# Performance work log

Hardware: AMD Instinct MI355X
Metric: run time of the kernel (lower is better)

## Reference

```python
import jax, jax.numpy as jnp
import numpy as np

B, L, X, Y, A = 32, 1024, 1024, 1024, 16


def setup_inputs() -> dict:
    key = jax.random.key(0)
    ks = jax.random.split(key, 6)
    stdv = 1.0 / np.sqrt(X)
    stdv_h = 1.0 / np.sqrt(Y)
    return {
        "x": jax.random.normal(ks[0], (B, L, X), dtype=jnp.float32),
        "y": jax.random.normal(ks[1], (B, Y), dtype=jnp.float32),
        "x_mask": jnp.zeros((B, L), dtype=bool),
        "actions": jax.random.randint(ks[2], (B,), 0, A),
        "weight": jax.random.uniform(ks[3], (Y, X), minval=-stdv, maxval=stdv, dtype=jnp.float32),
        "bias": jnp.zeros((X,), dtype=jnp.float32),
        "wa_h": jax.random.uniform(ks[4], (A, Y, 1), minval=-stdv_h, maxval=stdv_h, dtype=jnp.float32),
    }


def reference(x, y, x_mask, actions, weight, bias, wa_h):
    # Per-action column scores: softmax over x_size of sum_y(weight * wa_h[a])
    # (equivalent to the torch loop: a2 = weight*wa_h[a]; softmax(a2.sum(0)))
    score2 = jax.nn.softmax(jnp.einsum("yx,ay->ax", weight, wa_h[:, :, 0]), axis=-1)  # [A, X]
    # u[b,a,:] = y[b] @ (weight * score2[a]) = (y@weight)[b] * score2[a];
    # the one-hot mask then selects row actions[b] -> gather instead of A GEMMs.
    yW = y @ weight                                   # [B, X]
    Wy = yW * score2[actions] + bias                  # [B, X]
    xWy = jnp.einsum("blx,bx->bl", x, Wy)             # [B, L]
    xWy = jnp.where(x_mask, -jnp.inf, xWy)
    return jax.nn.log_softmax(xWy, axis=-1)  # training mode
```

## Files before the change

### kernel.cpp

```cpp
#include <hip/hip_runtime.h>
#include <hip/hip_bf16.h>
#include <math.h>

constexpr int Ac = 16;
constexpr int Bc = 32;
constexpr int Lc = 1024;
constexpr int Xc = 1024;
constexpr int Yc = 1024;

__device__ __forceinline__ float waveReduceSum(float v) {
#pragma unroll
    for (int off = 32; off > 0; off >>= 1) v += __shfl_down(v, off, 64);
    return v;
}

__device__ __forceinline__ float waveReduceMax(float v) {
#pragma unroll
    for (int off = 32; off > 0; off >>= 1) v = fmaxf(v, __shfl_down(v, off, 64));
    return v;
}

__global__ __launch_bounds__(256) void k1_proj(
        const float* __restrict__ weight, const float* __restrict__ yv,
        const float* __restrict__ wa_h, float* __restrict__ s_raw,
        float* __restrict__ yW) {
    const int x  = blockIdx.x * 256 + threadIdx.x;
    const int y0 = blockIdx.y * 64;

    float accA[Ac];
    float accB[Bc];
#pragma unroll
    for (int a = 0; a < Ac; ++a) accA[a] = 0.0f;
#pragma unroll
    for (int b = 0; b < Bc; ++b) accB[b] = 0.0f;

    for (int yy = 0; yy < 64; ++yy) {
        const int yi = y0 + yy;
        const float w = weight[(size_t)yi * Xc + x];
#pragma unroll
        for (int a = 0; a < Ac; ++a) accA[a] = fmaf(w, wa_h[a * Yc + yi], accA[a]);
#pragma unroll
        for (int b = 0; b < Bc; ++b) accB[b] = fmaf(w, yv[b * Yc + yi], accB[b]);
    }

#pragma unroll
    for (int a = 0; a < Ac; ++a) atomicAdd(&s_raw[a * Xc + x], accA[a]);
#pragma unroll
    for (int b = 0; b < Bc; ++b) atomicAdd(&yW[b * Xc + x], accB[b]);
}

__global__ __launch_bounds__(256) void k2_softmax(
        const float* __restrict__ s_raw, float* __restrict__ score2) {
    const int a    = blockIdx.x;
    const int tid  = threadIdx.x;
    const int wave = tid >> 6;
    const int lane = tid & 63;
    __shared__ float smax[4];
    __shared__ float ssum[4];

    float v[4];
    float mx = -INFINITY;
#pragma unroll
    for (int k = 0; k < 4; ++k) {
        v[k] = s_raw[a * Xc + tid + k * 256];
        mx = fmaxf(mx, v[k]);
    }
    mx = waveReduceMax(mx);
    if (lane == 0) smax[wave] = mx;
    __syncthreads();
    mx = fmaxf(fmaxf(smax[0], smax[1]), fmaxf(smax[2], smax[3]));

    float sum = 0.0f;
#pragma unroll
    for (int k = 0; k < 4; ++k) {
        v[k] = __expf(v[k] - mx);
        sum += v[k];
    }
    sum = waveReduceSum(sum);
    if (lane == 0) ssum[wave] = sum;
    __syncthreads();
    sum = ssum[0] + ssum[1] + ssum[2] + ssum[3];

    const float inv = 1.0f / sum;
#pragma unroll
    for (int k = 0; k < 4; ++k) score2[a * Xc + tid + k * 256] = v[k] * inv;
}

__global__ __launch_bounds__(256) void k3_dot(
        const float* __restrict__ x, const float* __restrict__ yW,
        const float* __restrict__ score2, const float* __restrict__ bias,
        const int* __restrict__ actions, float* __restrict__ xWy) {
    const int b  = blockIdx.y;
    const int l0 = blockIdx.x * 16;
    __shared__ float Wy[Xc];

    const int act = actions[b];
#pragma unroll
    for (int k = 0; k < 4; ++k) {
        const int xi = threadIdx.x + k * 256;
        Wy[xi] = fmaf(yW[b * Xc + xi], score2[act * Xc + xi], bias[xi]);
    }
    __syncthreads();

    const int wave = threadIdx.x >> 6;
    const int lane = threadIdx.x & 63;
    const float4* WyV = (const float4*)Wy;

    for (int r = wave; r < 16; r += 4) {
        const int l = l0 + r;
        const float4* xp = (const float4*)(x + ((size_t)b * Lc + l) * Xc);
        float acc = 0.0f;
#pragma unroll
        for (int k = 0; k < 4; ++k) {
            const int idx = lane + k * 64;
            const float4 xv = xp[idx];
            const float4 wv = WyV[idx];
            acc = fmaf(xv.x, wv.x, acc);
            acc = fmaf(xv.y, wv.y, acc);
            acc = fmaf(xv.z, wv.z, acc);
            acc = fmaf(xv.w, wv.w, acc);
        }
        acc = waveReduceSum(acc);
        if (lane == 0) xWy[b * Lc + l] = acc;
    }
}

__global__ __launch_bounds__(256) void k4_logsoftmax(
        const float* __restrict__ xWy, const unsigned char* __restrict__ mask,
        float* __restrict__ out) {
    const int b    = blockIdx.x;
    const int tid  = threadIdx.x;
    const int wave = tid >> 6;
    const int lane = tid & 63;
    __shared__ float smax[4];
    __shared__ float ssum[4];

    float v[4];
    float mx = -INFINITY;
#pragma unroll
    for (int k = 0; k < 4; ++k) {
        const int l = tid + k * 256;
        float t = xWy[b * Lc + l];
        if (mask[b * Lc + l]) t = -INFINITY;
        v[k] = t;
        mx = fmaxf(mx, t);
    }
    mx = waveReduceMax(mx);
    if (lane == 0) smax[wave] = mx;
    __syncthreads();
    mx = fmaxf(fmaxf(smax[0], smax[1]), fmaxf(smax[2], smax[3]));

    float sum = 0.0f;
#pragma unroll
    for (int k = 0; k < 4; ++k) sum += __expf(v[k] - mx);
    sum = waveReduceSum(sum);
    if (lane == 0) ssum[wave] = sum;
    __syncthreads();
    sum = ssum[0] + ssum[1] + ssum[2] + ssum[3];

    const float lse = mx + __logf(sum);
#pragma unroll
    for (int k = 0; k < 4; ++k) out[b * Lc + tid + k * 256] = v[k] - lse;
}

extern "C" void kernel_launch(void* const* d_in, const int* in_sizes, int n_in,
                              void* d_out, int out_size, void* d_ws, size_t ws_size,
                              hipStream_t stream) {
    const float* x          = (const float*)d_in[0];
    const float* yv         = (const float*)d_in[1];
    const unsigned char* xm = (const unsigned char*)d_in[2];
    const int* actions      = (const int*)d_in[3];
    const float* weight     = (const float*)d_in[4];
    const float* bias       = (const float*)d_in[5];
    const float* wa_h       = (const float*)d_in[6];
    float* out              = (float*)d_out;

    char* ws      = (char*)d_ws;
    float* s_raw  = (float*)(ws);
    float* score2 = (float*)(ws + 64 * 1024);
    float* yW     = (float*)(ws + 128 * 1024);
    float* xWy    = (float*)(ws + 256 * 1024);

    hipMemsetAsync(d_ws, 0, 256 * 1024, stream);

    k1_proj<<<dim3(Xc / 256, Yc / 64), 256, 0, stream>>>(weight, yv, wa_h, s_raw, yW);
    k2_softmax<<<Ac, 256, 0, stream>>>(s_raw, score2);
    k3_dot<<<dim3(Lc / 16, Bc), 256, 0, stream>>>(x, yW, score2, bias, actions, xWy);
    k4_logsoftmax<<<Bc, 256, 0, stream>>>(xWy, xm, out);
}
```

Before: 242.8 us.

## Split projection kernel over more Y tiles and stage coefficients in LDS

The projection kernel now processes 16 Y rows per block instead of 64, giving four times as many blocks to fill the GPU. The wa_h and y coefficients are staged in shared memory and read as float4 broadcasts, while weight values are preloaded into registers. The trade-off is four times as many atomic adds into the accumulators. The workspace layout is rearranged so that only the atomically accumulated buffers are zeroed.

```diff
diff --git a/kernel.cpp b/kernel.cpp
--- a/kernel.cpp
+++ b/kernel.cpp
@@ -7,6 +7,7 @@
 constexpr int Lc = 1024;
 constexpr int Xc = 1024;
 constexpr int Yc = 1024;
+constexpr int Cc = Ac + Bc;
 
 __device__ __forceinline__ float waveReduceSum(float v) {
 #pragma unroll
@@ -25,28 +26,46 @@
         const float* __restrict__ wa_h, float* __restrict__ s_raw,
         float* __restrict__ yW) {
     const int x  = blockIdx.x * 256 + threadIdx.x;
-    const int y0 = blockIdx.y * 64;
-
-    float accA[Ac];
-    float accB[Bc];
-#pragma unroll
-    for (int a = 0; a < Ac; ++a) accA[a] = 0.0f;
-#pragma unroll
-    for (int b = 0; b < Bc; ++b) accB[b] = 0.0f;
-
-    for (int yy = 0; yy < 64; ++yy) {
-        const int yi = y0 + yy;
-        const float w = weight[(size_t)yi * Xc + x];
-#pragma unroll
-        for (int a = 0; a < Ac; ++a) accA[a] = fmaf(w, wa_h[a * Yc + yi], accA[a]);
-#pragma unroll
-        for (int b = 0; b < Bc; ++b) accB[b] = fmaf(w, yv[b * Yc + yi], accB[b]);
-    }
-
-#pragma unroll
-    for (int a = 0; a < Ac; ++a) atomicAdd(&s_raw[a * Xc + x], accA[a]);
-#pragma unroll
-    for (int b = 0; b < Bc; ++b) atomicAdd(&yW[b * Xc + x], accB[b]);
+    const int y0 = blockIdx.y * 16;
+
+    __shared__ float cLDS[Cc][16];
+
+#pragma unroll
+    for (int k = 0; k < 3; ++k) {
+        const int idx = threadIdx.x + k * 256;
+        const int row = idx >> 4;
+        const int col = idx & 15;
+        cLDS[row][col] = (row < Ac) ? wa_h[row * Yc + y0 + col]
+                                    : yv[(row - Ac) * Yc + y0 + col];
+    }
+
+    float w[16];
+#pragma unroll
+    for (int t = 0; t < 16; ++t) w[t] = weight[(size_t)(y0 + t) * Xc + x];
+
+    __syncthreads();
+
+    float acc[Cc];
+#pragma unroll
+    for (int j = 0; j < Cc; ++j) acc[j] = 0.0f;
+
+    const float4* cvec = (const float4*)cLDS;
+#pragma unroll
+    for (int j = 0; j < Cc; ++j) {
+#pragma unroll
+        for (int q = 0; q < 4; ++q) {
+            const float4 c = cvec[j * 4 + q];
+            acc[j] = fmaf(w[q * 4 + 0], c.x, acc[j]);
+            acc[j] = fmaf(w[q * 4 + 1], c.y, acc[j]);
+            acc[j] = fmaf(w[q * 4 + 2], c.z, acc[j]);
+            acc[j] = fmaf(w[q * 4 + 3], c.w, acc[j]);
+        }
+    }
+
+#pragma unroll
+    for (int j = 0; j < Ac; ++j) atomicAdd(&s_raw[j * Xc + x], acc[j]);
+#pragma unroll
+    for (int j = Ac; j < Cc; ++j) atomicAdd(&yW[(j - Ac) * Xc + x], acc[j]);
 }
 
 __global__ __launch_bounds__(256) void k2_softmax(
@@ -177,13 +196,13 @@
 
     char* ws      = (char*)d_ws;
     float* s_raw  = (float*)(ws);
-    float* score2 = (float*)(ws + 64 * 1024);
-    float* yW     = (float*)(ws + 128 * 1024);
+    float* yW     = (float*)(ws + 64 * 1024);
+    float* score2 = (float*)(ws + 192 * 1024);
     float* xWy    = (float*)(ws + 256 * 1024);
 
-    hipMemsetAsync(d_ws, 0, 256 * 1024, stream);
-
-    k1_proj<<<dim3(Xc / 256, Yc / 64), 256, 0, stream>>>(weight, yv, wa_h, s_raw, yW);
+    hipMemsetAsync(d_ws, 0, 192 * 1024, stream);
+
+    k1_proj<<<dim3(Xc / 256, Yc / 16), 256, 0, stream>>>(weight, yv, wa_h, s_raw, yW);
     k2_softmax<<<Ac, 256, 0, stream>>>(s_raw, score2);
     k3_dot<<<dim3(Lc / 16, Bc), 256, 0, stream>>>(x, yW, score2, bias, actions, xWy);
     k4_logsoftmax<<<Bc, 256, 0, stream>>>(xWy, xm, out);
```

Result: faster. 223.8 us (-7.8%).
